# Performance work log

Hardware: AMD Instinct MI355X
Metric: run time of the kernel (lower is better)

## Reference

```python
import jax, jax.numpy as jnp
import numpy as np

H = 4  # num_heads
K = 16  # model_k
EPS = 1e-5


def layernorm(x, g, b):
    m = jnp.mean(x, axis=-1, keepdims=True)
    v = jnp.mean(jnp.square(x - m), axis=-1, keepdims=True)
    return (x - m) * jax.lax.rsqrt(v + EPS) * g + b


def setup_inputs() -> dict:
    key = jax.random.key(0)
    ks = jax.random.split(key, 12)
    B, N, C, NN = 4, 8192, 256, 32
    s = 0.02
    return {
        "xyz": jax.random.normal(ks[0], (B, N, 2), jnp.float32),
        "xy_embed": jax.random.normal(ks[1], (B, N, C), jnp.float32),
        "nns": jax.random.randint(ks[2], (B, N, NN), 0, N),
        "ln1_g": jnp.ones((C,), jnp.float32),
        "ln1_b": jnp.zeros((C,), jnp.float32),
        "w_qkv": jax.random.normal(ks[3], (C, 3 * C), jnp.float32) * s,
        "w_d1": jax.random.normal(ks[4], (2, C), jnp.float32) * s,
        "b_d1": jnp.zeros((C,), jnp.float32),
        "w_d2": jax.random.normal(ks[5], (C, C), jnp.float32) * s,
        "b_d2": jnp.zeros((C,), jnp.float32),
        "w_proj": jax.random.normal(ks[6], (C, C), jnp.float32) * s,
        "b_proj": jnp.zeros((C,), jnp.float32),
        "ln2_g": jnp.ones((C,), jnp.float32),
        "ln2_b": jnp.zeros((C,), jnp.float32),
        "w_m1": jax.random.normal(ks[7], (C, 4 * C), jnp.float32) * s,
        "b_m1": jnp.zeros((4 * C,), jnp.float32),
        "w_m2": jax.random.normal(ks[8], (4 * C, C), jnp.float32) * s,
        "b_m2": jnp.zeros((C,), jnp.float32),
    }


def reference(xyz, xy_embed, nns, ln1_g, ln1_b, w_qkv, w_d1, b_d1, w_d2, b_d2,
              w_proj, b_proj, ln2_g, ln2_b, w_m1, b_m1, w_m2, b_m2):
    B, N, C = xy_embed.shape
    hd = C // H
    knn = nns[:, :, :K]  # [B, N, K]
    bidx = jnp.arange(B)[:, None, None]

    # --- Attention on norm1(xy_embed) ---
    h = layernorm(xy_embed, ln1_g, ln1_b)
    qkv = h @ w_qkv  # [B, N, 3C]
    q, kf, vf = jnp.split(qkv, 3, axis=-1)

    kk = kf[bidx, knn]  # gather: [B, N, K, C]
    vv = vf[bidx, knn]  # [B, N, K, C]
    xy_knn = xyz[bidx, knn]  # [B, N, K, 2]

    # relative position encoding MLP
    rel = xyz[:, :, None, :] - xy_knn  # [B, N, K, 2]
    pe = jax.nn.relu(rel @ w_d1 + b_d1) @ w_d2 + b_d2  # [B, N, K, C]

    # split heads (channel-chunk split, matching torch reshape semantics)
    qh = q.reshape(B, N, H, hd).transpose(0, 2, 1, 3)          # [B,H,N,hd]
    kh = kk.reshape(B, N, K, H, hd).transpose(0, 3, 1, 2, 4)   # [B,H,N,K,hd]
    vh = vv.reshape(B, N, K, H, hd).transpose(0, 3, 1, 2, 4)
    peh = pe.reshape(B, N, K, H, hd).transpose(0, 3, 1, 2, 4)

    attn = jnp.einsum('bhnd,bhnkd->bhnk', qh, kh) / np.sqrt(hd).astype(np.float32)
    attn = jax.nn.softmax(attn, axis=-1)  # [B,H,N,K]

    x = jnp.einsum('bhnk,bhnkd->bhnd', attn, vh + peh)  # [B,H,N,hd]
    x = x.transpose(0, 2, 1, 3).reshape(B, N, C)
    x = x @ w_proj + b_proj

    # residual + MLP block
    x = xy_embed + x
    h2 = layernorm(x, ln2_g, ln2_b)
    mlp = jax.nn.gelu(h2 @ w_m1 + b_m1, approximate=False) @ w_m2 + b_m2
    x = x + mlp
    return x
```

## Files before the change

### kernel.cpp

```cpp
#include <hip/hip_runtime.h>
#include <hip/hip_bf16.h>
#include <math.h>

#define NPTS 8192
#define BDIM 4
#define BN   32768
#define CDIM 256
#define KNN  16
#define NNCOL 32

typedef __attribute__((ext_vector_type(8))) short short8_t;
typedef __attribute__((ext_vector_type(4))) float f32x4;

__device__ __forceinline__ ushort bf16_rne(float f) {
  unsigned int u = __float_as_uint(f);
  u += 0x7fffu + ((u >> 16) & 1u);
  return (ushort)(u >> 16);
}
__device__ __forceinline__ void bf16_split(float f, ushort& h, ushort& l) {
  unsigned int u = __float_as_uint(f);
  h = (ushort)(u >> 16);
  float fh = __uint_as_float(u & 0xffff0000u);
  l = (ushort)(__float_as_uint(f - fh) >> 16);
}
__device__ __forceinline__ float bf16_tof(ushort h) {
  return __uint_as_float(((unsigned int)h) << 16);
}
__device__ __forceinline__ float gelu_exact(float z) {
  return 0.5f * z * (1.0f + erff(z * 0.70710678118654752f));
}

__global__ __launch_bounds__(256) void wsplit_kernel(
    const float* __restrict__ in, ushort* __restrict__ oh,
    ushort* __restrict__ ol, int R, int Cc) {
  __shared__ float tile[32][33];
  const int tx = threadIdx.x & 31, ty = threadIdx.x >> 5;
  const int r0 = blockIdx.y * 32, c0 = blockIdx.x * 32;
  #pragma unroll
  for (int i = 0; i < 4; i++)
    tile[ty + 8 * i][tx] = in[(size_t)(r0 + ty + 8 * i) * Cc + c0 + tx];
  __syncthreads();
  #pragma unroll
  for (int i = 0; i < 4; i++) {
    const int cc = ty + 8 * i;
    ushort h, l;
    bf16_split(tile[tx][cc], h, l);
    oh[(size_t)(c0 + cc) * R + r0 + tx] = h;
    ol[(size_t)(c0 + cc) * R + r0 + tx] = l;
  }
}

__global__ __launch_bounds__(256) void ln_apply_kernel(
    const float* __restrict__ x, const float* __restrict__ g,
    const float* __restrict__ b, ushort* __restrict__ oh,
    ushort* __restrict__ ol) {
  const int row = blockIdx.x * 4 + (threadIdx.x >> 6);
  const int l = threadIdx.x & 63;
  const float4 v = *(const float4*)(x + (size_t)row * CDIM + l * 4);
  float s  = v.x + v.y + v.z + v.w;
  float sq = v.x * v.x + v.y * v.y + v.z * v.z + v.w * v.w;
  #pragma unroll
  for (int off = 1; off < 64; off <<= 1) {
    s  += __shfl_xor(s, off);
    sq += __shfl_xor(sq, off);
  }
  const float m = s * (1.0f / 256.0f);
  const float r = rsqrtf(sq * (1.0f / 256.0f) - m * m + 1e-5f);
  const float4 gv = *(const float4*)(g + l * 4);
  const float4 bv = *(const float4*)(b + l * 4);
  const float y0 = (v.x - m) * r * gv.x + bv.x;
  const float y1 = (v.y - m) * r * gv.y + bv.y;
  const float y2 = (v.z - m) * r * gv.z + bv.z;
  const float y3 = (v.w - m) * r * gv.w + bv.w;
  ushort4 hv, lv;
  bf16_split(y0, hv.x, lv.x); bf16_split(y1, hv.y, lv.y);
  bf16_split(y2, hv.z, lv.z); bf16_split(y3, hv.w, lv.w);
  *(ushort4*)(oh + (size_t)row * CDIM + l * 4) = hv;
  *(ushort4*)(ol + (size_t)row * CDIM + l * 4) = lv;
}

template <int EPI>
__global__ __launch_bounds__(256) void gemm_bf3(
    const ushort* __restrict__ AH, const ushort* __restrict__ AL,
    const ushort* __restrict__ BH, const ushort* __restrict__ BL,
    const float* __restrict__ bias, float* __restrict__ Cf,
    ushort* __restrict__ CH, ushort* __restrict__ CL,
    const float* __restrict__ res, int M, int Nn, int Kk) {
  __shared__ __align__(16) ushort AsH[128 * 32];
  __shared__ __align__(16) ushort AsL[128 * 32];
  __shared__ __align__(16) ushort BsH[128 * 32];
  __shared__ __align__(16) ushort BsL[128 * 32];

  const int t = threadIdx.x;
  const int w = t >> 6;
  const int l = t & 63;
  const int la = l & 15;
  const int lb = l >> 4;
  const int wr = w >> 1;
  const int wc = w & 1;
  const int m0 = blockIdx.y * 128;
  const int n0 = blockIdx.x * 128;

  f32x4 acc[4][4];
  #pragma unroll
  for (int i = 0; i < 4; i++)
    #pragma unroll
    for (int j = 0; j < 4; j++) acc[i][j] = (f32x4){0.f, 0.f, 0.f, 0.f};

  for (int k0 = 0; k0 < Kk; k0 += 32) {
    #pragma unroll
    for (int gi = 0; gi < 2; gi++) {
      const int g = t + gi * 256;
      const int row = g >> 2;
      const int kg = (g & 3) * 8;
      const int lds_off = row * 32 + (kg ^ ((row & 3) << 3));
      const size_t ga = (size_t)(m0 + row) * Kk + k0 + kg;
      const size_t gb = (size_t)(n0 + row) * Kk + k0 + kg;
      *(short8_t*)&AsH[lds_off] = *(const short8_t*)(AH + ga);
      *(short8_t*)&AsL[lds_off] = *(const short8_t*)(AL + ga);
      *(short8_t*)&BsH[lds_off] = *(const short8_t*)(BH + gb);
      *(short8_t*)&BsL[lds_off] = *(const short8_t*)(BL + gb);
    }
    __syncthreads();

    short8_t aH[4], aL[4], bH[4], bL[4];
    #pragma unroll
    for (int i = 0; i < 4; i++) {
      const int row = wr * 64 + i * 16 + la;
      const int off = row * 32 + ((lb * 8) ^ ((row & 3) << 3));
      aH[i] = *(const short8_t*)&AsH[off];
      aL[i] = *(const short8_t*)&AsL[off];
    }
    #pragma unroll
    for (int j = 0; j < 4; j++) {
      const int row = wc * 64 + j * 16 + la;
      const int off = row * 32 + ((lb * 8) ^ ((row & 3) << 3));
      bH[j] = *(const short8_t*)&BsH[off];
      bL[j] = *(const short8_t*)&BsL[off];
    }
    #pragma unroll
    for (int i = 0; i < 4; i++)
      #pragma unroll
      for (int j = 0; j < 4; j++) {
        acc[i][j] = __builtin_amdgcn_mfma_f32_16x16x32_bf16(aH[i], bH[j], acc[i][j], 0, 0, 0);
        acc[i][j] = __builtin_amdgcn_mfma_f32_16x16x32_bf16(aH[i], bL[j], acc[i][j], 0, 0, 0);
        acc[i][j] = __builtin_amdgcn_mfma_f32_16x16x32_bf16(aL[i], bH[j], acc[i][j], 0, 0, 0);
      }
    __syncthreads();
  }

  const int colBase = n0 + wc * 64 + la;
  float biasv[4] = {0.f, 0.f, 0.f, 0.f};
  if (EPI >= 2) {
    #pragma unroll
    for (int j = 0; j < 4; j++) biasv[j] = bias[colBase + j * 16];
  }
  #pragma unroll
  for (int i = 0; i < 4; i++) {
    #pragma unroll
    for (int r = 0; r < 4; r++) {
      const int row = m0 + wr * 64 + i * 16 + lb * 4 + r;
      #pragma unroll
      for (int j = 0; j < 4; j++) {
        const int col = colBase + j * 16;
        float o = acc[i][j][r] + biasv[j];
        if (EPI == 0) {
          CH[(size_t)row * Nn + col] = bf16_rne(o);
        } else if (EPI == 2) {
          o += res[(size_t)row * Nn + col];
          Cf[(size_t)row * Nn + col] = o;
        } else {
          o = gelu_exact(o);
          ushort h, lo2;
          bf16_split(o, h, lo2);
          CH[(size_t)row * Nn + col] = h;
          CL[(size_t)row * Nn + col] = lo2;
        }
      }
    }
  }
}

__global__ __launch_bounds__(256) void attn_kernel(
    const ushort* __restrict__ qkv, const int* __restrict__ nns,
    const float* __restrict__ xyz, const float* __restrict__ w_d1,
    const float* __restrict__ b_d1, const float* __restrict__ w_d2,
    const float* __restrict__ b_d2, ushort* __restrict__ outH,
    ushort* __restrict__ outL) {
  __shared__ __align__(16) float s_lds[8][4][256];
  __shared__ __align__(16) float ov_lds[8][256];
  __shared__ float a_lds[8][64];

  const int t = threadIdx.x;
  const int w = t >> 6;
  const int l = t & 63;
  const int h = l >> 4;
  const int c0 = l * 4;
  const int blk = blockIdx.x;

  const float4 w10 = *(const float4*)(w_d1 + c0);
  const float4 w11 = *(const float4*)(w_d1 + 256 + c0);
  const float4 b1v = *(const float4*)(b_d1 + c0);
  const float4 b2v = *(const float4*)(b_d2 + c0);

  for (int pl = 0; pl < 2; pl++) {
    const int p  = w * 2 + pl;
    const int gp = blk * 8 + p;
    const int b  = gp >> 13;

    const ushort4 qu = *(const ushort4*)(qkv + (size_t)gp * 768 + c0);
    const float q0 = bf16_tof(qu.x), q1 = bf16_tof(qu.y);
    const float q2 = bf16_tof(qu.z), q3 = bf16_tof(qu.w);
    const float2 xy0 = *(const float2*)(xyz + gp * 2);

    int rowj[KNN];
    #pragma unroll
    for (int j = 0; j < KNN; j++) rowj[j] = (b << 13) + nns[gp * NNCOL + j];

    float myscore = 0.f;
    #pragma unroll
    for (int j = 0; j < KNN; j++) {
      const ushort4 ku = *(const ushort4*)(qkv + (size_t)rowj[j] * 768 + 256 + c0);
      float d = q0 * bf16_tof(ku.x) + q1 * bf16_tof(ku.y) +
                q2 * bf16_tof(ku.z) + q3 * bf16_tof(ku.w);
      d += __shfl_xor(d, 1); d += __shfl_xor(d, 2);
      d += __shfl_xor(d, 4); d += __shfl_xor(d, 8);
      if ((l & 15) == j) myscore = d;
    }
    myscore *= 0.125f;

    float mx = myscore;
    mx = fmaxf(mx, __shfl_xor(mx, 1)); mx = fmaxf(mx, __shfl_xor(mx, 2));
    mx = fmaxf(mx, __shfl_xor(mx, 4)); mx = fmaxf(mx, __shfl_xor(mx, 8));
    float e = __expf(myscore - mx);
    float sum = e;
    sum += __shfl_xor(sum, 1); sum += __shfl_xor(sum, 2);
    sum += __shfl_xor(sum, 4); sum += __shfl_xor(sum, 8);
    const float a = e / sum;
    a_lds[p][l] = a;
    __syncthreads();

    float sacc[4][4] = {};
    float4 ov = {0.f, 0.f, 0.f, 0.f};
    #pragma unroll
    for (int j = 0; j < KNN; j++) {
      const int r = rowj[j];
      const ushort4 vu = *(const ushort4*)(qkv + (size_t)r * 768 + 512 + c0);
      const float v0 = bf16_tof(vu.x), v1 = bf16_tof(vu.y);
      const float v2 = bf16_tof(vu.z), v3 = bf16_tof(vu.w);
      const float2 xyj = *(const float2*)(xyz + r * 2);
      const float rx = xy0.x - xyj.x;
      const float ry = xy0.y - xyj.y;
      const float u0 = fmaxf(rx * w10.x + ry * w11.x + b1v.x, 0.f);
      const float u1 = fmaxf(rx * w10.y + ry * w11.y + b1v.y, 0.f);
      const float u2 = fmaxf(rx * w10.z + ry * w11.z + b1v.z, 0.f);
      const float u3 = fmaxf(rx * w10.w + ry * w11.w + b1v.w, 0.f);
      const float a0 = a_lds[p][0 * 16 + j];
      const float a1 = a_lds[p][1 * 16 + j];
      const float a2 = a_lds[p][2 * 16 + j];
      const float a3 = a_lds[p][3 * 16 + j];
      sacc[0][0] += a0 * u0; sacc[0][1] += a0 * u1; sacc[0][2] += a0 * u2; sacc[0][3] += a0 * u3;
      sacc[1][0] += a1 * u0; sacc[1][1] += a1 * u1; sacc[1][2] += a1 * u2; sacc[1][3] += a1 * u3;
      sacc[2][0] += a2 * u0; sacc[2][1] += a2 * u1; sacc[2][2] += a2 * u2; sacc[2][3] += a2 * u3;
      sacc[3][0] += a3 * u0; sacc[3][1] += a3 * u1; sacc[3][2] += a3 * u2; sacc[3][3] += a3 * u3;
      const float aown = (h < 2) ? (h == 0 ? a0 : a1) : (h == 2 ? a2 : a3);
      ov.x += aown * v0; ov.y += aown * v1;
      ov.z += aown * v2; ov.w += aown * v3;
    }
    #pragma unroll
    for (int hh = 0; hh < 4; hh++) {
      float4 sv;
      sv.x = sacc[hh][0]; sv.y = sacc[hh][1];
      sv.z = sacc[hh][2]; sv.w = sacc[hh][3];
      *(float4*)&s_lds[p][hh][c0] = sv;
    }
    float4 ovw;
    ovw.x = ov.x + b2v.x; ovw.y = ov.y + b2v.y;
    ovw.z = ov.z + b2v.z; ovw.w = ov.w + b2v.w;
    *(float4*)&ov_lds[p][c0] = ovw;
  }
  __syncthreads();

  const int d  = t;
  const int hh = d >> 6;
  float acc2[8];
  #pragma unroll
  for (int p = 0; p < 8; p++) acc2[p] = ov_lds[p][d];

  for (int c = 0; c < 256; c += 4) {
    const float wv0 = w_d2[(c + 0) * 256 + d];
    const float wv1 = w_d2[(c + 1) * 256 + d];
    const float wv2 = w_d2[(c + 2) * 256 + d];
    const float wv3 = w_d2[(c + 3) * 256 + d];
    #pragma unroll
    for (int p = 0; p < 8; p++) {
      const float4 s4 = *(const float4*)&s_lds[p][hh][c];
      acc2[p] += s4.x * wv0 + s4.y * wv1 + s4.z * wv2 + s4.w * wv3;
    }
  }
  const int gp0 = blk * 8;
  #pragma unroll
  for (int p = 0; p < 8; p++) {
    ushort hv, lv;
    bf16_split(acc2[p], hv, lv);
    outH[(size_t)(gp0 + p) * 256 + d] = hv;
    outL[(size_t)(gp0 + p) * 256 + d] = lv;
  }
}

extern "C" void kernel_launch(void* const* d_in, const int* in_sizes, int n_in,
                              void* d_out, int out_size, void* d_ws,
                              size_t ws_size, hipStream_t stream) {
  const float* xyz      = (const float*)d_in[0];
  const float* xy_embed = (const float*)d_in[1];
  const int*   nns      = (const int*)d_in[2];
  const float* ln1_g    = (const float*)d_in[3];
  const float* ln1_b    = (const float*)d_in[4];
  const float* w_qkv    = (const float*)d_in[5];
  const float* w_d1     = (const float*)d_in[6];
  const float* b_d1     = (const float*)d_in[7];
  const float* w_d2     = (const float*)d_in[8];
  const float* b_d2     = (const float*)d_in[9];
  const float* w_proj   = (const float*)d_in[10];
  const float* b_proj   = (const float*)d_in[11];
  const float* ln2_g    = (const float*)d_in[12];
  const float* ln2_b    = (const float*)d_in[13];
  const float* w_m1     = (const float*)d_in[14];
  const float* b_m1     = (const float*)d_in[15];
  const float* w_m2     = (const float*)d_in[16];
  const float* b_m2     = (const float*)d_in[17];
  float* out = (float*)d_out;

  char* ws = (char*)d_ws;
  const size_t MB = 1024 * 1024;
  ushort* qkv_bf = (ushort*)(ws);
  ushort* midH   = (ushort*)(ws);
  ushort* midL   = (ushort*)(ws + 32 * MB);
  ushort* attnH  = (ushort*)(ws + 48 * MB);
  ushort* attnL  = (ushort*)(ws + 64 * MB);
  ushort* lnH    = (ushort*)(ws + 80 * MB);
  ushort* lnL    = (ushort*)(ws + 96 * MB);
  ushort* wbase  = (ushort*)(ws + 112 * MB);
  ushort* WqH  = wbase;            ushort* WqL  = WqH + 768 * 256;
  ushort* WpH  = WqL + 768 * 256;  ushort* WpL  = WpH + 256 * 256;
  ushort* Wm1H = WpL + 256 * 256;  ushort* Wm1L = Wm1H + 1024 * 256;
  ushort* Wm2H = Wm1L + 1024 * 256; ushort* Wm2L = Wm2H + 256 * 1024;

  wsplit_kernel<<<dim3(768 / 32, 256 / 32), 256, 0, stream>>>(w_qkv, WqH, WqL, 256, 768);
  wsplit_kernel<<<dim3(256 / 32, 256 / 32), 256, 0, stream>>>(w_proj, WpH, WpL, 256, 256);
  wsplit_kernel<<<dim3(1024 / 32, 256 / 32), 256, 0, stream>>>(w_m1, Wm1H, Wm1L, 256, 1024);
  wsplit_kernel<<<dim3(256 / 32, 1024 / 32), 256, 0, stream>>>(w_m2, Wm2H, Wm2L, 1024, 256);

  ln_apply_kernel<<<BN / 4, 256, 0, stream>>>(xy_embed, ln1_g, ln1_b, lnH, lnL);

  gemm_bf3<0><<<dim3(768 / 128, BN / 128), 256, 0, stream>>>(
      lnH, lnL, WqH, WqL, nullptr, nullptr, qkv_bf, nullptr, nullptr, BN, 768, 256);

  attn_kernel<<<BN / 8, 256, 0, stream>>>(qkv_bf, nns, xyz, w_d1, b_d1, w_d2,
                                          b_d2, attnH, attnL);

  gemm_bf3<2><<<dim3(256 / 128, BN / 128), 256, 0, stream>>>(
      attnH, attnL, WpH, WpL, b_proj, out, nullptr, nullptr, xy_embed, BN, 256, 256);

  ln_apply_kernel<<<BN / 4, 256, 0, stream>>>(out, ln2_g, ln2_b, lnH, lnL);

  const int CHUNK = 16384;
  for (int ch = 0; ch < BN / CHUNK; ch++) {
    float* xrow = out + (size_t)ch * CHUNK * 256;
    gemm_bf3<3><<<dim3(1024 / 128, CHUNK / 128), 256, 0, stream>>>(
        lnH + (size_t)ch * CHUNK * 256, lnL + (size_t)ch * CHUNK * 256,
        Wm1H, Wm1L, b_m1, nullptr, midH, midL, nullptr, CHUNK, 1024, 256);
    gemm_bf3<2><<<dim3(256 / 128, CHUNK / 128), 256, 0, stream>>>(
        midH, midL, Wm2H, Wm2L, b_m2, xrow, nullptr, nullptr, xrow, CHUNK, 256, 1024);
  }
}
```

Measured before the change: 603.4 us.

## Use bf16 MFMA for PE second-layer matmul and vectorize QK score computation

Replaces the scalar fp32 per-point w_d2 matmul in the attention kernel with bf16 MFMA 16x16x32 instructions. The attention-weighted relu features go into a swizzled LDS tile as bf16, and the weights come from a new pre-split bf16 copy of w_d2. The QK score loop is restructured so each lane computes one neighbor's full head dot product with 16-byte vector loads, replacing the per-neighbor shuffle reductions. This removes a large scalar FMA loop and many shuffles, at the cost of bf16 rounding of both PE-matmul operands (only the high part is used) and an extra weight-split launch.

```diff
diff --git a/kernel.cpp b/kernel.cpp
--- a/kernel.cpp
+++ b/kernel.cpp
@@ -184,10 +184,10 @@
 __global__ __launch_bounds__(256) void attn_kernel(
     const ushort* __restrict__ qkv, const int* __restrict__ nns,
     const float* __restrict__ xyz, const float* __restrict__ w_d1,
-    const float* __restrict__ b_d1, const float* __restrict__ w_d2,
+    const float* __restrict__ b_d1, const ushort* __restrict__ W2H,
     const float* __restrict__ b_d2, ushort* __restrict__ outH,
     ushort* __restrict__ outL) {
-  __shared__ __align__(16) float s_lds[8][4][256];
+  __shared__ __align__(16) ushort s_lds[32 * 256];
   __shared__ __align__(16) float ov_lds[8][256];
   __shared__ float a_lds[8][64];
 
@@ -195,6 +195,7 @@
   const int w = t >> 6;
   const int l = t & 63;
   const int h = l >> 4;
+  const int j16 = l & 15;
   const int c0 = l * 4;
   const int blk = blockIdx.x;
 
@@ -208,36 +209,33 @@
     const int gp = blk * 8 + p;
     const int b  = gp >> 13;
 
-    const ushort4 qu = *(const ushort4*)(qkv + (size_t)gp * 768 + c0);
-    const float q0 = bf16_tof(qu.x), q1 = bf16_tof(qu.y);
-    const float q2 = bf16_tof(qu.z), q3 = bf16_tof(qu.w);
     const float2 xy0 = *(const float2*)(xyz + gp * 2);
 
     int rowj[KNN];
     #pragma unroll
     for (int j = 0; j < KNN; j++) rowj[j] = (b << 13) + nns[gp * NNCOL + j];
 
-    float myscore = 0.f;
-    #pragma unroll
-    for (int j = 0; j < KNN; j++) {
-      const ushort4 ku = *(const ushort4*)(qkv + (size_t)rowj[j] * 768 + 256 + c0);
-      float d = q0 * bf16_tof(ku.x) + q1 * bf16_tof(ku.y) +
-                q2 * bf16_tof(ku.z) + q3 * bf16_tof(ku.w);
-      d += __shfl_xor(d, 1); d += __shfl_xor(d, 2);
-      d += __shfl_xor(d, 4); d += __shfl_xor(d, 8);
-      if ((l & 15) == j) myscore = d;
-    }
-    myscore *= 0.125f;
+    const size_t qbase = (size_t)gp * 768 + (h << 6);
+    const size_t kbase = (size_t)rowj[j16] * 768 + 256 + (h << 6);
+    float d = 0.f;
+    #pragma unroll
+    for (int u = 0; u < 8; u++) {
+      const short8_t qv = *(const short8_t*)(qkv + qbase + u * 8);
+      const short8_t kv = *(const short8_t*)(qkv + kbase + u * 8);
+      #pragma unroll
+      for (int e = 0; e < 8; e++)
+        d += bf16_tof((ushort)qv[e]) * bf16_tof((ushort)kv[e]);
+    }
+    const float myscore = d * 0.125f;
 
     float mx = myscore;
     mx = fmaxf(mx, __shfl_xor(mx, 1)); mx = fmaxf(mx, __shfl_xor(mx, 2));
     mx = fmaxf(mx, __shfl_xor(mx, 4)); mx = fmaxf(mx, __shfl_xor(mx, 8));
-    float e = __expf(myscore - mx);
+    const float e = __expf(myscore - mx);
     float sum = e;
     sum += __shfl_xor(sum, 1); sum += __shfl_xor(sum, 2);
     sum += __shfl_xor(sum, 4); sum += __shfl_xor(sum, 8);
-    const float a = e / sum;
-    a_lds[p][l] = a;
+    a_lds[p][l] = e / sum;
     __syncthreads();
 
     float sacc[4][4] = {};
@@ -263,16 +261,17 @@
       sacc[1][0] += a1 * u0; sacc[1][1] += a1 * u1; sacc[1][2] += a1 * u2; sacc[1][3] += a1 * u3;
       sacc[2][0] += a2 * u0; sacc[2][1] += a2 * u1; sacc[2][2] += a2 * u2; sacc[2][3] += a2 * u3;
       sacc[3][0] += a3 * u0; sacc[3][1] += a3 * u1; sacc[3][2] += a3 * u2; sacc[3][3] += a3 * u3;
-      const float aown = (h < 2) ? (h == 0 ? a0 : a1) : (h == 2 ? a2 : a3);
+      const float aown = a_lds[p][(h << 4) + j];
       ov.x += aown * v0; ov.y += aown * v1;
       ov.z += aown * v2; ov.w += aown * v3;
     }
     #pragma unroll
     for (int hh = 0; hh < 4; hh++) {
-      float4 sv;
-      sv.x = sacc[hh][0]; sv.y = sacc[hh][1];
-      sv.z = sacc[hh][2]; sv.w = sacc[hh][3];
-      *(float4*)&s_lds[p][hh][c0] = sv;
+      const int row = p * 4 + hh;
+      ushort4 sv;
+      sv.x = bf16_rne(sacc[hh][0]); sv.y = bf16_rne(sacc[hh][1]);
+      sv.z = bf16_rne(sacc[hh][2]); sv.w = bf16_rne(sacc[hh][3]);
+      *(ushort4*)&s_lds[row * 256 + (c0 ^ ((row & 15) << 3))] = sv;
     }
     float4 ovw;
     ovw.x = ov.x + b2v.x; ovw.y = ov.y + b2v.y;
@@ -281,30 +280,54 @@
   }
   __syncthreads();
 
-  const int d  = t;
-  const int hh = d >> 6;
-  float acc2[8];
-  #pragma unroll
-  for (int p = 0; p < 8; p++) acc2[p] = ov_lds[p][d];
-
-  for (int c = 0; c < 256; c += 4) {
-    const float wv0 = w_d2[(c + 0) * 256 + d];
-    const float wv1 = w_d2[(c + 1) * 256 + d];
-    const float wv2 = w_d2[(c + 2) * 256 + d];
-    const float wv3 = w_d2[(c + 3) * 256 + d];
-    #pragma unroll
-    for (int p = 0; p < 8; p++) {
-      const float4 s4 = *(const float4*)&s_lds[p][hh][c];
-      acc2[p] += s4.x * wv0 + s4.y * wv1 + s4.z * wv2 + s4.w * wv3;
-    }
-  }
-  const int gp0 = blk * 8;
-  #pragma unroll
-  for (int p = 0; p < 8; p++) {
-    ushort hv, lv;
-    bf16_split(acc2[p], hv, lv);
-    outH[(size_t)(gp0 + p) * 256 + d] = hv;
-    outL[(size_t)(gp0 + p) * 256 + d] = lv;
+  const int la = l & 15;
+  const int lb = l >> 4;
+  f32x4 acc2[2][4];
+  #pragma unroll
+  for (int mf = 0; mf < 2; mf++)
+    #pragma unroll
+    for (int nf = 0; nf < 4; nf++) acc2[mf][nf] = (f32x4){0.f, 0.f, 0.f, 0.f};
+
+  #pragma unroll
+  for (int ks = 0; ks < 8; ks++) {
+    const int k8 = lb * 8 + ks * 32;
+    short8_t av[2], bv[4];
+    #pragma unroll
+    for (int mf = 0; mf < 2; mf++) {
+      const int row = mf * 16 + la;
+      av[mf] = *(const short8_t*)&s_lds[row * 256 + (k8 ^ ((row & 15) << 3))];
+    }
+    #pragma unroll
+    for (int nf = 0; nf < 4; nf++) {
+      const int n = (w << 6) + nf * 16 + la;
+      bv[nf] = *(const short8_t*)(W2H + (size_t)n * 256 + k8);
+    }
+    #pragma unroll
+    for (int mf = 0; mf < 2; mf++)
+      #pragma unroll
+      for (int nf = 0; nf < 4; nf++)
+        acc2[mf][nf] = __builtin_amdgcn_mfma_f32_16x16x32_bf16(
+            av[mf], bv[nf], acc2[mf][nf], 0, 0, 0);
+  }
+
+  #pragma unroll
+  for (int mf = 0; mf < 2; mf++) {
+    const int p = mf * 4 + lb;
+    const size_t gp = (size_t)(blk * 8 + p);
+    #pragma unroll
+    for (int nf = 0; nf < 4; nf++) {
+      const int c = (w << 6) + nf * 16 + la;
+      float pe;
+      if (w == 0)      pe = acc2[mf][nf][0];
+      else if (w == 1) pe = acc2[mf][nf][1];
+      else if (w == 2) pe = acc2[mf][nf][2];
+      else             pe = acc2[mf][nf][3];
+      const float o = pe + ov_lds[p][c];
+      ushort hv, lv;
+      bf16_split(o, hv, lv);
+      outH[gp * 256 + c] = hv;
+      outL[gp * 256 + c] = lv;
+    }
   }
 }
 
@@ -341,22 +364,24 @@
   ushort* lnH    = (ushort*)(ws + 80 * MB);
   ushort* lnL    = (ushort*)(ws + 96 * MB);
   ushort* wbase  = (ushort*)(ws + 112 * MB);
-  ushort* WqH  = wbase;            ushort* WqL  = WqH + 768 * 256;
-  ushort* WpH  = WqL + 768 * 256;  ushort* WpL  = WpH + 256 * 256;
-  ushort* Wm1H = WpL + 256 * 256;  ushort* Wm1L = Wm1H + 1024 * 256;
+  ushort* WqH  = wbase;             ushort* WqL  = WqH + 768 * 256;
+  ushort* WpH  = WqL + 768 * 256;   ushort* WpL  = WpH + 256 * 256;
+  ushort* Wm1H = WpL + 256 * 256;   ushort* Wm1L = Wm1H + 1024 * 256;
   ushort* Wm2H = Wm1L + 1024 * 256; ushort* Wm2L = Wm2H + 256 * 1024;
+  ushort* W2H  = Wm2L + 256 * 1024; ushort* W2L  = W2H + 256 * 256;
 
   wsplit_kernel<<<dim3(768 / 32, 256 / 32), 256, 0, stream>>>(w_qkv, WqH, WqL, 256, 768);
   wsplit_kernel<<<dim3(256 / 32, 256 / 32), 256, 0, stream>>>(w_proj, WpH, WpL, 256, 256);
   wsplit_kernel<<<dim3(1024 / 32, 256 / 32), 256, 0, stream>>>(w_m1, Wm1H, Wm1L, 256, 1024);
   wsplit_kernel<<<dim3(256 / 32, 1024 / 32), 256, 0, stream>>>(w_m2, Wm2H, Wm2L, 1024, 256);
+  wsplit_kernel<<<dim3(256 / 32, 256 / 32), 256, 0, stream>>>(w_d2, W2H, W2L, 256, 256);
 
   ln_apply_kernel<<<BN / 4, 256, 0, stream>>>(xy_embed, ln1_g, ln1_b, lnH, lnL);
 
   gemm_bf3<0><<<dim3(768 / 128, BN / 128), 256, 0, stream>>>(
       lnH, lnL, WqH, WqL, nullptr, nullptr, qkv_bf, nullptr, nullptr, BN, 768, 256);
 
-  attn_kernel<<<BN / 8, 256, 0, stream>>>(qkv_bf, nns, xyz, w_d1, b_d1, w_d2,
+  attn_kernel<<<BN / 8, 256, 0, stream>>>(qkv_bf, nns, xyz, w_d1, b_d1, W2H,
                                           b_d2, attnH, attnL);
 
   gemm_bf3<2><<<dim3(256 / 128, BN / 128), 256, 0, stream>>>(
```

Result: no change. 611.1 us (+1.3%).
